# Kernel tuning notes

Measured on AMD Instinct MI355X. Metric: run time of the kernel, lower is better.

The kernel has to match this reference:

```python
import jax, jax.numpy as jnp
import numpy as np

NUM_ITERATIONS = 3


def squash(t, axis=-1):
    # scale * t / sqrt(||t||^2 + eps), scale = ||t||^2 / (1 + ||t||^2)
    sq = jnp.sum(t * t, axis=axis, keepdims=True)
    return (sq / (1.0 + sq)) * t / jnp.sqrt(sq + 1e-8)


def setup_inputs() -> dict:
    key = jax.random.key(0)
    k1, k2 = jax.random.split(key)
    B, C, R, I, O = 128, 10, 8192, 8, 16
    x = jax.random.normal(k1, (B, R, I), dtype=jnp.float32)
    route_weights = jax.random.normal(k2, (C, R, I, O), dtype=jnp.float32) * 0.1
    return {"x": x, "route_weights": route_weights}


def reference(x, route_weights):
    # x: [B, R, I]; route_weights: [C, R, I, O]
    u_hat = jnp.einsum('bri,crio->bcro', x, route_weights)  # [B, C, R, O]
    B, C, R, O = u_hat.shape
    b_ij = jnp.zeros((B, C, R), dtype=u_hat.dtype)
    v_j = None
    for it in range(NUM_ITERATIONS):
        c_ij = jax.nn.softmax(b_ij, axis=1)                 # [B, C, R]
        s_j = jnp.einsum('bcr,bcro->bco', c_ij, u_hat)      # [B, C, O]
        v_j = squash(s_j, axis=-1)                          # [B, C, O]
        if it < NUM_ITERATIONS - 1:
            a_ij = jnp.einsum('bcro,bco->bcr', u_hat, v_j)  # [B, C, R]
            b_ij = b_ij + a_ij
    return v_j
```

## Files before the change

### kernel.cpp

```cpp
#include <hip/hip_runtime.h>
#include <hip/hip_fp16.h>
#include <math.h>

#define B_ 128
#define C_ 10
#define R_ 8192
#define I_ 8
#define O_ 16

typedef __attribute__((ext_vector_type(8))) _Float16 half8;
typedef __attribute__((ext_vector_type(16))) float f32x16;

#define XROW 512
#define WROW 64
#define WZERO 80
#define SBO (C_ * B_ * O_)

__device__ __forceinline__ unsigned pk2(float a, float b) {
    __half2 h = __floats2half2_rn(a, b);
    return *(unsigned*)&h;
}

__global__ __launch_bounds__(256, 4) void fused_iter(const float* __restrict__ x,
                                                     const float* __restrict__ w,
                                                     const float* __restrict__ vsum,
                                                     __half* __restrict__ part,
                                                     int mode) {
    __shared__ unsigned xls[8 * XROW];
    __shared__ unsigned wls[(80 + 1) * WROW];

    const int tid = threadIdx.x;
    const int wave = tid >> 6;
    const int lane = tid & 63;
    const int n = lane & 31;
    const int g = lane >> 5;
    const int rp_m = (lane & 31) >> 4;
    const int o_m = lane & 15;
    const int b = wave * 32 + n;
    const int r0 = blockIdx.x * 8;

#pragma unroll
    for (int k = 0; k < 8; ++k) {
        const int f = k * 256 + tid;
        const int bb = f >> 4;
        const int rr = (f >> 1) & 7;
        const int q = f & 1;
        const float4 v = *(const float4*)(x + ((size_t)bb * R_ + r0 + rr) * 8 + q * 4);
        *(uint2*)(xls + rr * XROW + bb * 4 + q * 2) = make_uint2(pk2(v.x, v.y), pk2(v.z, v.w));
    }
#pragma unroll
    for (int k = 0; k < 5; ++k) {
        const int id = k * 256 + tid;
        const int o = id & 15;
        const int r = (id >> 4) & 7;
        const int c = id >> 7;
        const float* wp = w + ((size_t)(c * R_ + r0 + r) * 8) * 16 + o;
        const float f0 = wp[0],  f1 = wp[16],  f2 = wp[32],  f3 = wp[48];
        const float f4 = wp[64], f5 = wp[80],  f6 = wp[96],  f7 = wp[112];
        *(uint4*)(wls + (c * 8 + r) * WROW + o * 4) =
            make_uint4(pk2(f0, f1), pk2(f2, f3), pk2(f4, f5), pk2(f6, f7));
    }
    if (tid < WROW) wls[WZERO * WROW + tid] = 0u;
    __syncthreads();

    float dacc[8];
#pragma unroll
    for (int j = 0; j < 8; ++j) dacc[j] = 0.f;

    const int act = (g == rp_m);

    if (mode) {
#pragma unroll 1
        for (int c = 0; c < C_; ++c) {
            const float4* vp = (const float4*)(vsum + ((size_t)c * B_ + b) * O_ + 4 * g);
            const float4 va = vp[0];
            const float4 vb = vp[2];
#pragma unroll
            for (int rp = 0; rp < 4; ++rp) {
                const int woff = act ? ((c * 8 + 2 * rp + g) * WROW + o_m * 4)
                                     : (WZERO * WROW);
                const half8 a  = *(const half8*)(wls + woff);
                const half8 xb = *(const half8*)(xls + (2 * rp + g) * XROW + b * 4);
                f32x16 u;
#pragma unroll
                for (int j = 0; j < 16; ++j) u[j] = 0.f;
                u = __builtin_amdgcn_mfma_f32_32x32x16_f16(a, xb, u, 0, 0, 0);
                float p0 = u[0] * va.x + u[1] * va.y + u[2] * va.z + u[3] * va.w
                         + u[4] * vb.x + u[5] * vb.y + u[6] * vb.z + u[7] * vb.w;
                float p1 = u[8] * va.x + u[9] * va.y + u[10] * va.z + u[11] * va.w
                         + u[12] * vb.x + u[13] * vb.y + u[14] * vb.z + u[15] * vb.w;
                p0 += __shfl_xor(p0, 32);
                p1 += __shfl_xor(p1, 32);
                dacc[2 * rp]     += __expf(p0);
                dacc[2 * rp + 1] += __expf(p1);
            }
        }
#pragma unroll
        for (int j = 0; j < 8; ++j) dacc[j] = 1.0f / dacc[j];
    }

#pragma unroll 1
    for (int c = 0; c < C_; ++c) {
        float4 va, vb;
        if (mode) {
            const float4* vp = (const float4*)(vsum + ((size_t)c * B_ + b) * O_ + 4 * g);
            va = vp[0]; vb = vp[2];
        }
        f32x16 acc;
#pragma unroll
        for (int j = 0; j < 16; ++j) acc[j] = 0.f;

#pragma unroll
        for (int rp = 0; rp < 4; ++rp) {
            const int woff = act ? ((c * 8 + 2 * rp + g) * WROW + o_m * 4)
                                 : (WZERO * WROW);
            const half8 a  = *(const half8*)(wls + woff);
            const half8 xb = *(const half8*)(xls + (2 * rp + g) * XROW + b * 4);
            f32x16 u;
#pragma unroll
            for (int j = 0; j < 16; ++j) u[j] = 0.f;
            u = __builtin_amdgcn_mfma_f32_32x32x16_f16(a, xb, u, 0, 0, 0);
            float c0, c1;
            if (mode) {
                float p0 = u[0] * va.x + u[1] * va.y + u[2] * va.z + u[3] * va.w
                         + u[4] * vb.x + u[5] * vb.y + u[6] * vb.z + u[7] * vb.w;
                float p1 = u[8] * va.x + u[9] * va.y + u[10] * va.z + u[11] * va.w
                         + u[12] * vb.x + u[13] * vb.y + u[14] * vb.z + u[15] * vb.w;
                p0 += __shfl_xor(p0, 32);
                p1 += __shfl_xor(p1, 32);
                c0 = __expf(p0) * dacc[2 * rp];
                c1 = __expf(p1) * dacc[2 * rp + 1];
            } else {
                c0 = 0.1f; c1 = 0.1f;
            }
#pragma unroll
            for (int j = 0; j < 8; ++j)  acc[j] += c0 * u[j];
#pragma unroll
            for (int j = 8; j < 16; ++j) acc[j] += c1 * u[j];
        }

        const float f0 = acc[0] + acc[8],  f1 = acc[1] + acc[9];
        const float f2 = acc[2] + acc[10], f3 = acc[3] + acc[11];
        const float f4 = acc[4] + acc[12], f5 = acc[5] + acc[13];
        const float f6 = acc[6] + acc[14], f7 = acc[7] + acc[15];
        __half* pp = part + (((size_t)blockIdx.x * C_ + c) * B_ + b) * O_;
        *(uint2*)(pp + 4 * g)     = make_uint2(pk2(f0, f1), pk2(f2, f3));
        *(uint2*)(pp + 8 + 4 * g) = make_uint2(pk2(f4, f5), pk2(f6, f7));
    }
}

__global__ __launch_bounds__(256) void reduce1(const __half* __restrict__ part,
                                               float* __restrict__ part2) {
    const int t = blockIdx.x * 256 + threadIdx.x;
    const int s0 = blockIdx.y * 64;
    const __half* p = part + (size_t)s0 * SBO + t;
    float sum = 0.f;
#pragma unroll 8
    for (int s = 0; s < 64; ++s)
        sum += __half2float(p[(size_t)s * SBO]);
    part2[(size_t)blockIdx.y * SBO + t] = sum;
}

__global__ __launch_bounds__(256) void finish_pass(const float* __restrict__ part2,
                                                   float* __restrict__ vsum,
                                                   float* __restrict__ out,
                                                   int mode) {
    const int t = blockIdx.x * 256 + threadIdx.x;
    float sum = 0.f;
#pragma unroll
    for (int s = 0; s < 16; ++s)
        sum += part2[(size_t)s * SBO + t];

    float sq = sum * sum;
    sq += __shfl_xor(sq, 1);
    sq += __shfl_xor(sq, 2);
    sq += __shfl_xor(sq, 4);
    sq += __shfl_xor(sq, 8);
    const float scale = sq / ((1.0f + sq) * sqrtf(sq + 1e-8f));
    const float v = scale * sum;

    if (mode == 0) {
        vsum[t] = v;
    } else if (mode == 1) {
        vsum[t] += v;
    } else {
        const int o = t & 15, b = (t >> 4) & 127, c = t >> 11;
        out[((size_t)b * C_ + c) * O_ + o] = v;
    }
}

extern "C" void kernel_launch(void* const* d_in, const int* in_sizes, int n_in,
                              void* d_out, int out_size, void* d_ws, size_t ws_size,
                              hipStream_t stream) {
    const float* x = (const float*)d_in[0];
    const float* w = (const float*)d_in[1];
    float* out = (float*)d_out;

    __half* part = (__half*)d_ws;
    float* part2 = (float*)(part + (size_t)1024 * SBO);
    float* vsum  = part2 + (size_t)16 * SBO;

    const dim3 fgrid(R_ / 8);
    const dim3 rgrid(80, 16);
    const dim3 ggrid(80);

    fused_iter<<<fgrid, 256, 0, stream>>>(x, w, vsum, part, 0);
    reduce1<<<rgrid, 256, 0, stream>>>(part, part2);
    finish_pass<<<ggrid, 256, 0, stream>>>(part2, vsum, out, 0);

    fused_iter<<<fgrid, 256, 0, stream>>>(x, w, vsum, part, 1);
    reduce1<<<rgrid, 256, 0, stream>>>(part, part2);
    finish_pass<<<ggrid, 256, 0, stream>>>(part2, vsum, out, 1);

    fused_iter<<<fgrid, 256, 0, stream>>>(x, w, vsum, part, 1);
    reduce1<<<rgrid, 256, 0, stream>>>(part, part2);
    finish_pass<<<ggrid, 256, 0, stream>>>(part2, vsum, out, 2);
}
```

Before: 227.5 us.

## Cache routing exponentials across passes, simplify first iteration, vectorize partial reduction

In the routing passes, the exponentials of the agreement logits from the first pass (softmax denominator) are now kept in registers and reused in the second pass. This removes the recomputation of the dot products with v, the cross-lane shuffles and the exp calls, and each lane now computes only its own half of the shuffle pair. The first iteration now accumulates through the MFMA accumulator with a constant 0.1 scale instead of doing per-element FMAs. The partial-sum reduction kernel reads 8 halves per thread with 16-byte loads and runs on a smaller grid. The cost is more register pressure from the e[10][4] array and full unrolling, which may reduce occupancy.

```diff
diff --git a/kernel.cpp b/kernel.cpp
--- a/kernel.cpp
+++ b/kernel.cpp
@@ -63,102 +63,125 @@
     if (tid < WROW) wls[WZERO * WROW + tid] = 0u;
     __syncthreads();
 
-    float dacc[8];
-#pragma unroll
-    for (int j = 0; j < 8; ++j) dacc[j] = 0.f;
-
     const int act = (g == rp_m);
 
+    f32x16 zero16;
+#pragma unroll
+    for (int j = 0; j < 16; ++j) zero16[j] = 0.f;
+
     if (mode) {
-#pragma unroll 1
+        float e[C_][4];
+        float dinv[4];
+        {
+            float dacc[4] = {0.f, 0.f, 0.f, 0.f};
+#pragma unroll
+            for (int c = 0; c < C_; ++c) {
+                const float4* vp = (const float4*)(vsum + ((size_t)c * B_ + b) * O_ + 4 * g);
+                const float4 va = vp[0];
+                const float4 vb = vp[2];
+#pragma unroll
+                for (int rp = 0; rp < 4; ++rp) {
+                    const int woff = act ? ((c * 8 + 2 * rp + g) * WROW + o_m * 4)
+                                         : (WZERO * WROW);
+                    const half8 a  = *(const half8*)(wls + woff);
+                    const half8 xb = *(const half8*)(xls + (2 * rp + g) * XROW + b * 4);
+                    const f32x16 u = __builtin_amdgcn_mfma_f32_32x32x16_f16(a, xb, zero16, 0, 0, 0);
+                    const float p0 = u[0] * va.x + u[1] * va.y + u[2] * va.z + u[3] * va.w
+                                   + u[4] * vb.x + u[5] * vb.y + u[6] * vb.z + u[7] * vb.w;
+                    const float p1 = u[8] * va.x + u[9] * va.y + u[10] * va.z + u[11] * va.w
+                                   + u[12] * vb.x + u[13] * vb.y + u[14] * vb.z + u[15] * vb.w;
+                    const float send = g ? p0 : p1;
+                    const float recv = __shfl_xor(send, 32);
+                    const float pg = (g ? p1 : p0) + recv;
+                    const float ee = __expf(pg);
+                    e[c][rp] = ee;
+                    dacc[rp] += ee;
+                }
+            }
+#pragma unroll
+            for (int rp = 0; rp < 4; ++rp) dinv[rp] = 1.0f / dacc[rp];
+        }
+
+#pragma unroll
         for (int c = 0; c < C_; ++c) {
-            const float4* vp = (const float4*)(vsum + ((size_t)c * B_ + b) * O_ + 4 * g);
-            const float4 va = vp[0];
-            const float4 vb = vp[2];
+            f32x16 acc;
 #pragma unroll
             for (int rp = 0; rp < 4; ++rp) {
                 const int woff = act ? ((c * 8 + 2 * rp + g) * WROW + o_m * 4)
                                      : (WZERO * WROW);
                 const half8 a  = *(const half8*)(wls + woff);
                 const half8 xb = *(const half8*)(xls + (2 * rp + g) * XROW + b * 4);
-                f32x16 u;
-#pragma unroll
-                for (int j = 0; j < 16; ++j) u[j] = 0.f;
-                u = __builtin_amdgcn_mfma_f32_32x32x16_f16(a, xb, u, 0, 0, 0);
-                float p0 = u[0] * va.x + u[1] * va.y + u[2] * va.z + u[3] * va.w
-                         + u[4] * vb.x + u[5] * vb.y + u[6] * vb.z + u[7] * vb.w;
-                float p1 = u[8] * va.x + u[9] * va.y + u[10] * va.z + u[11] * va.w
-                         + u[12] * vb.x + u[13] * vb.y + u[14] * vb.z + u[15] * vb.w;
-                p0 += __shfl_xor(p0, 32);
-                p1 += __shfl_xor(p1, 32);
-                dacc[2 * rp]     += __expf(p0);
-                dacc[2 * rp + 1] += __expf(p1);
+                const f32x16 u = __builtin_amdgcn_mfma_f32_32x32x16_f16(a, xb, zero16, 0, 0, 0);
+                const float w_own = e[c][rp] * dinv[rp];
+                const float w_oth = __shfl_xor(w_own, 32);
+                const float c0 = g ? w_oth : w_own;
+                const float c1 = g ? w_own : w_oth;
+                if (rp == 0) {
+#pragma unroll
+                    for (int j = 0; j < 8; ++j)  acc[j] = c0 * u[j];
+#pragma unroll
+                    for (int j = 8; j < 16; ++j) acc[j] = c1 * u[j];
+                } else {
+#pragma unroll
+                    for (int j = 0; j < 8; ++j)  acc[j] += c0 * u[j];
+#pragma unroll
+                    for (int j = 8; j < 16; ++j) acc[j] += c1 * u[j];
+                }
             }
+            const float f0 = acc[0] + acc[8],  f1 = acc[1] + acc[9];
+            const float f2 = acc[2] + acc[10], f3 = acc[3] + acc[11];
+            const float f4 = acc[4] + acc[12], f5 = acc[5] + acc[13];
+            const float f6 = acc[6] + acc[14], f7 = acc[7] + acc[15];
+            __half* pp = part + (((size_t)blockIdx.x * C_ + c) * B_ + b) * O_;
+            *(uint2*)(pp + 4 * g)     = make_uint2(pk2(f0, f1), pk2(f2, f3));
+            *(uint2*)(pp + 8 + 4 * g) = make_uint2(pk2(f4, f5), pk2(f6, f7));
         }
-#pragma unroll
-        for (int j = 0; j < 8; ++j) dacc[j] = 1.0f / dacc[j];
-    }
-
-#pragma unroll 1
-    for (int c = 0; c < C_; ++c) {
-        float4 va, vb;
-        if (mode) {
-            const float4* vp = (const float4*)(vsum + ((size_t)c * B_ + b) * O_ + 4 * g);
-            va = vp[0]; vb = vp[2];
+    } else {
+#pragma unroll
+        for (int c = 0; c < C_; ++c) {
+            f32x16 acc = zero16;
+#pragma unroll
+            for (int rp = 0; rp < 4; ++rp) {
+                const int woff = act ? ((c * 8 + 2 * rp + g) * WROW + o_m * 4)
+                                     : (WZERO * WROW);
+                const half8 a  = *(const half8*)(wls + woff);
+                const half8 xb = *(const half8*)(xls + (2 * rp + g) * XROW + b * 4);
+                acc = __builtin_amdgcn_mfma_f32_32x32x16_f16(a, xb, acc, 0, 0, 0);
+            }
+            const float f0 = (acc[0] + acc[8])  * 0.1f, f1 = (acc[1] + acc[9])  * 0.1f;
+            const float f2 = (acc[2] + acc[10]) * 0.1f, f3 = (acc[3] + acc[11]) * 0.1f;
+            const float f4 = (acc[4] + acc[12]) * 0.1f, f5 = (acc[5] + acc[13]) * 0.1f;
+            const float f6 = (acc[6] + acc[14]) * 0.1f, f7 = (acc[7] + acc[15]) * 0.1f;
+            __half* pp = part + (((size_t)blockIdx.x * C_ + c) * B_ + b) * O_;
+            *(uint2*)(pp + 4 * g)     = make_uint2(pk2(f0, f1), pk2(f2, f3));
+            *(uint2*)(pp + 8 + 4 * g) = make_uint2(pk2(f4, f5), pk2(f6, f7));
         }
-        f32x16 acc;
-#pragma unroll
-        for (int j = 0; j < 16; ++j) acc[j] = 0.f;
-
-#pragma unroll
-        for (int rp = 0; rp < 4; ++rp) {
-            const int woff = act ? ((c * 8 + 2 * rp + g) * WROW + o_m * 4)
-                                 : (WZERO * WROW);
-            const half8 a  = *(const half8*)(wls + woff);
-            const half8 xb = *(const half8*)(xls + (2 * rp + g) * XROW + b * 4);
-            f32x16 u;
-#pragma unroll
-            for (int j = 0; j < 16; ++j) u[j] = 0.f;
-            u = __builtin_amdgcn_mfma_f32_32x32x16_f16(a, xb, u, 0, 0, 0);
-            float c0, c1;
-            if (mode) {
-                float p0 = u[0] * va.x + u[1] * va.y + u[2] * va.z + u[3] * va.w
-                         + u[4] * vb.x + u[5] * vb.y + u[6] * vb.z + u[7] * vb.w;
-                float p1 = u[8] * va.x + u[9] * va.y + u[10] * va.z + u[11] * va.w
-                         + u[12] * vb.x + u[13] * vb.y + u[14] * vb.z + u[15] * vb.w;
-                p0 += __shfl_xor(p0, 32);
-                p1 += __shfl_xor(p1, 32);
-                c0 = __expf(p0) * dacc[2 * rp];
-                c1 = __expf(p1) * dacc[2 * rp + 1];
-            } else {
-                c0 = 0.1f; c1 = 0.1f;
-            }
-#pragma unroll
-            for (int j = 0; j < 8; ++j)  acc[j] += c0 * u[j];
-#pragma unroll
-            for (int j = 8; j < 16; ++j) acc[j] += c1 * u[j];
-        }
-
-        const float f0 = acc[0] + acc[8],  f1 = acc[1] + acc[9];
-        const float f2 = acc[2] + acc[10], f3 = acc[3] + acc[11];
-        const float f4 = acc[4] + acc[12], f5 = acc[5] + acc[13];
-        const float f6 = acc[6] + acc[14], f7 = acc[7] + acc[15];
-        __half* pp = part + (((size_t)blockIdx.x * C_ + c) * B_ + b) * O_;
-        *(uint2*)(pp + 4 * g)     = make_uint2(pk2(f0, f1), pk2(f2, f3));
-        *(uint2*)(pp + 8 + 4 * g) = make_uint2(pk2(f4, f5), pk2(f6, f7));
     }
 }
 
 __global__ __launch_bounds__(256) void reduce1(const __half* __restrict__ part,
                                                float* __restrict__ part2) {
-    const int t = blockIdx.x * 256 + threadIdx.x;
-    const int s0 = blockIdx.y * 64;
-    const __half* p = part + (size_t)s0 * SBO + t;
-    float sum = 0.f;
+    const int t8 = blockIdx.x * 256 + threadIdx.x;
+    const __half* p = part + (size_t)(blockIdx.y * 64) * SBO + (size_t)t8 * 8;
+    float s0 = 0.f, s1 = 0.f, s2 = 0.f, s3 = 0.f;
+    float s4 = 0.f, s5 = 0.f, s6 = 0.f, s7 = 0.f;
 #pragma unroll 8
-    for (int s = 0; s < 64; ++s)
-        sum += __half2float(p[(size_t)s * SBO]);
-    part2[(size_t)blockIdx.y * SBO + t] = sum;
+    for (int s = 0; s < 64; ++s) {
+        const uint4 v = *(const uint4*)(p + (size_t)s * SBO);
+        const __half2 h0 = *(const __half2*)&v.x;
+        const __half2 h1 = *(const __half2*)&v.y;
+        const __half2 h2 = *(const __half2*)&v.z;
+        const __half2 h3 = *(const __half2*)&v.w;
+        const float2 f0 = __half22float2(h0);
+        const float2 f1 = __half22float2(h1);
+        const float2 f2 = __half22float2(h2);
+        const float2 f3 = __half22float2(h3);
+        s0 += f0.x; s1 += f0.y; s2 += f1.x; s3 += f1.y;
+        s4 += f2.x; s5 += f2.y; s6 += f3.x; s7 += f3.y;
+    }
+    float* q = part2 + (size_t)blockIdx.y * SBO + (size_t)t8 * 8;
+    *(float4*)q       = make_float4(s0, s1, s2, s3);
+    *(float4*)(q + 4) = make_float4(s4, s5, s6, s7);
 }
 
 __global__ __launch_bounds__(256) void finish_pass(const float* __restrict__ part2,
@@ -201,7 +224,7 @@
     float* vsum  = part2 + (size_t)16 * SBO;
 
     const dim3 fgrid(R_ / 8);
-    const dim3 rgrid(80, 16);
+    const dim3 rgrid(10, 16);
     const dim3 ggrid(80);
 
     fused_iter<<<fgrid, 256, 0, stream>>>(x, w, vsum, part, 0);
```

Result: slower. 318.0 us (+39.8%).
